# Kernel optimization log

Measured on AMD Instinct MI355X. Metric: run time of the kernel, lower is better.

## Reference

```python
import jax, jax.numpy as jnp
import numpy as np

BITS = 16          # number of histogram bins == number of spiking time steps
B, IN_DIM, HID = 16384, 784, 128


def setup_inputs() -> dict:
    key = jax.random.key(0)
    ks = jax.random.split(key, 9)
    dims = [(HID, IN_DIM), (HID, HID), (HID, HID), (IN_DIM, HID)]
    inp = {"features": jax.random.uniform(ks[0], (B, IN_DIM), jnp.float32)}
    for i, (o, d) in enumerate(dims):
        inp["W%d" % i] = jax.random.normal(ks[1 + i], (o, d), jnp.float32) * 0.05
        inp["b%d" % i] = jax.random.normal(ks[5 + i], (o,), jnp.float32) * 0.05
    # np.histogram_bin_edges(bins=16) -> 17 uniformly spaced edges per layer
    in_max = [1.0, 4.0, 4.0, 4.0]
    out_max = [4.0, 4.0, 4.0, 4.0]
    for i in range(4):
        inp["in_bins%d" % i] = jnp.linspace(0.0, in_max[i], BITS + 1, dtype=jnp.float32)
        inp["out_bins%d" % i] = jnp.linspace(0.0, out_max[i], BITS + 1, dtype=jnp.float32)
    return inp


def _spike(t):
    # output[output>1]=1; output[output<1]=0  (==1 stays 1)  -> (t >= 1)
    # totals[output==1] -= 1
    s = (t >= 1.0).astype(t.dtype)
    return s, t - s


def _forward(features, Ws, bs, in_bins, out_bins):
    h_in = [e[1] - e[0] for e in in_bins]    # uniform spike heights
    h_out = [e[1] - e[0] for e in out_bins]
    # set_up_weights: weight *= h_in; weight /= h_out (bias likewise)
    Weff = [Ws[l] * (h_in[l] / h_out[l]) for l in range(4)]
    beff = [bs[l] * (h_in[l] / h_out[l]) for l in range(4)]
    n = features.shape[0]
    # discretize: np.digitize(x, in_bins) - 1, then / 16.0 (non-differentiable)
    act = (jnp.digitize(jax.lax.stop_gradient(features), in_bins[0]) - 1).astype(features.dtype) / BITS
    t_in = jnp.zeros_like(features)                               # input-layer membrane
    totals = tuple(jnp.broadcast_to(beff[l], (n,) + beff[l].shape) for l in range(4))  # reset_totals: totals = bias
    out_acc = jnp.zeros((n, Weff[3].shape[0]), features.dtype)

    def step(carry, _):
        t_in, t0, t1, t2, t3, out = carry
        s_in, t_in = _spike(t_in + act)
        # process_layer: totals += sum(weight * spikes, axis=1) == spikes @ W.T
        s0, t0 = _spike(t0 + s_in @ Weff[0].T)
        s1, t1 = _spike(t1 + s0 @ Weff[1].T)
        s2, t2 = _spike(t2 + s1 @ Weff[2].T)
        s3, t3 = _spike(t3 + s2 @ Weff[3].T)
        return (t_in, t0, t1, t2, t3, out + s3), None

    carry, _ = jax.lax.scan(step, (t_in,) + totals + (out_acc,), None, length=BITS)
    out_spikes = carry[-1]
    # decoder_output_layer.reconstruct: spikes * (out_bins[1] - out_bins[0])
    return out_spikes * h_out[3]


def reference(features, W0, W1, W2, W3, b0, b1, b2, b3,
              in_bins0, in_bins1, in_bins2, in_bins3,
              out_bins0, out_bins1, out_bins2, out_bins3):
    return _forward(features,
                    [W0, W1, W2, W3], [b0, b1, b2, b3],
                    [in_bins0, in_bins1, in_bins2, in_bins3],
                    [out_bins0, out_bins1, out_bins2, out_bins3])
```

## Files before the change

### kernel.cpp

```cpp
#include <hip/hip_runtime.h>

#define IN_DIM 784
#define HID 128
#define NSTEP 16
#define BATCH 16384

constexpr int W0T_OFF = 0;
constexpr int W1T_OFF = W0T_OFF + IN_DIM*HID;
constexpr int W2T_OFF = W1T_OFF + HID*HID;
constexpr int W3T_OFF = W2T_OFF + HID*HID;
constexpr int B0_OFF  = W3T_OFF + HID*IN_DIM;
constexpr int B1_OFF  = B0_OFF + HID;
constexpr int B2_OFF  = B1_OFF + HID;
constexpr int B3_OFF  = B2_OFF + HID;
constexpr int WS_FLOATS = B3_OFF + IN_DIM;

constexpr int CHUNK_COLS = 32;
constexpr int CHUNK_F    = CHUNK_COLS * HID;
constexpr int NCHUNK     = 25;

__global__ __launch_bounds__(256) void prep_kernel(
    const float* __restrict__ W0, const float* __restrict__ b0,
    const float* __restrict__ W1, const float* __restrict__ b1,
    const float* __restrict__ W2, const float* __restrict__ b2,
    const float* __restrict__ W3, const float* __restrict__ b3,
    const float* __restrict__ ib0, const float* __restrict__ ob0,
    const float* __restrict__ ib1, const float* __restrict__ ob1,
    const float* __restrict__ ib2, const float* __restrict__ ob2,
    const float* __restrict__ ib3, const float* __restrict__ ob3,
    float* __restrict__ ws)
{
    int idx = blockIdx.x * 256 + threadIdx.x;
    if (idx >= WS_FLOATS) return;
    float r0 = (ib0[1] - ib0[0]) / (ob0[1] - ob0[0]);
    float r1 = (ib1[1] - ib1[0]) / (ob1[1] - ob1[0]);
    float r2 = (ib2[1] - ib2[0]) / (ob2[1] - ob2[0]);
    float r3 = (ib3[1] - ib3[0]) / (ob3[1] - ob3[0]);
    if (idx < W1T_OFF) {
        int t = idx;            int k = t >> 7, j = t & 127;
        ws[idx] = W0[j * IN_DIM + k] * r0;
    } else if (idx < W2T_OFF) {
        int t = idx - W1T_OFF;  int k = t >> 7, j = t & 127;
        ws[idx] = W1[j * HID + k] * r1;
    } else if (idx < W3T_OFF) {
        int t = idx - W2T_OFF;  int k = t >> 7, j = t & 127;
        ws[idx] = W2[j * HID + k] * r2;
    } else if (idx < B0_OFF) {
        int t = idx - W3T_OFF;  int k = t / IN_DIM, o = t % IN_DIM;
        ws[idx] = W3[o * HID + k] * r3;
    } else if (idx < B1_OFF) ws[idx] = b0[idx - B0_OFF] * r0;
    else if (idx < B2_OFF)   ws[idx] = b1[idx - B1_OFF] * r1;
    else if (idx < B3_OFF)   ws[idx] = b2[idx - B2_OFF] * r2;
    else                     ws[idx] = b3[idx - B3_OFF] * r3;
}

__global__ __launch_bounds__(256) void snn_main(
    const float* __restrict__ feat,
    const float* __restrict__ ws,
    const float* __restrict__ ib0,
    const float* __restrict__ ob3,
    float* __restrict__ out)
{
    __shared__ float smem[2 * CHUNK_F];

    const int tid  = threadIdx.x;
    const int lane = tid & 63;
    const int wid  = tid >> 6;
    const int sample = blockIdx.x * 4 + wid;

    const float* W0t = ws + W0T_OFF;
    const float* W1t = ws + W1T_OFF;
    const float* W2t = ws + W2T_OFF;
    const float* W3t = ws + W3T_OFF;
    const float* frow = feat + (size_t)sample * IN_DIM;

    float edge[16];
#pragma unroll
    for (int e = 0; e < 16; ++e) edge[e] = ib0[e + 1];

    {
        const float4* g4 = (const float4*)W0t;
        float4* lb = (float4*)smem;
#pragma unroll
        for (int i = 0; i < 4; ++i) lb[i * 256 + tid] = g4[i * 256 + tid];
    }
    __syncthreads();

    float2 C[16];
#pragma unroll
    for (int mv = 0; mv < 16; ++mv) C[mv] = make_float2(0.f, 0.f);

    for (int c = 0; c < NCHUNK; ++c) {
        float4 rg0, rg1, rg2, rg3;
        {
            const float4* g4 = (const float4*)W0t + (size_t)(c + 1) * (CHUNK_F / 4);
            rg0 = g4[0 * 256 + tid];
            rg1 = g4[1 * 256 + tid];
            rg2 = g4[2 * 256 + tid];
            rg3 = g4[3 * 256 + tid];
        }

        int col = c * CHUNK_COLS + (lane & 31);
        bool valid = col < IN_DIM;
        float x = frow[valid ? col : 0];
        int mm = 0;
#pragma unroll
        for (int e = 0; e < 16; ++e) mm += (x >= edge[e]) ? 1 : 0;
        if (!valid) mm = -1;

        const float2* bufp = (const float2*)(smem + (c & 1) * CHUNK_F);
#pragma unroll
        for (int mv = 1; mv <= 16; ++mv) {
            unsigned mk = (unsigned)__ballot(mm == mv);
            float2 ca = make_float2(0.f, 0.f), cb = make_float2(0.f, 0.f);
            while (mk) {
                int b0 = __builtin_ctz(mk); mk &= mk - 1;
                float2 w0 = bufp[b0 * 64 + lane];
                if (mk) {
                    int b1 = __builtin_ctz(mk); mk &= mk - 1;
                    float2 w1 = bufp[b1 * 64 + lane];
                    if (mk) {
                        int b2 = __builtin_ctz(mk); mk &= mk - 1;
                        float2 w2 = bufp[b2 * 64 + lane];
                        if (mk) {
                            int b3i = __builtin_ctz(mk); mk &= mk - 1;
                            float2 w3 = bufp[b3i * 64 + lane];
                            cb.x += w3.x; cb.y += w3.y;
                        }
                        ca.x += w2.x; ca.y += w2.y;
                    }
                    cb.x += w1.x; cb.y += w1.y;
                }
                ca.x += w0.x; ca.y += w0.y;
            }
            C[mv - 1].x += ca.x + cb.x;
            C[mv - 1].y += ca.y + cb.y;
        }

        if (c + 1 < NCHUNK) {
            float4* lb = (float4*)(smem + ((c + 1) & 1) * CHUNK_F);
            lb[0 * 256 + tid] = rg0;
            lb[1 * 256 + tid] = rg1;
            lb[2 * 256 + tid] = rg2;
            lb[3 * 256 + tid] = rg3;
        }
        __syncthreads();
    }

    float2 t0 = ((const float2*)(ws + B0_OFF))[lane];
    float2 t1 = ((const float2*)(ws + B1_OFF))[lane];
    float2 t2 = ((const float2*)(ws + B2_OFF))[lane];
    float4 t3[4], cnt[4];
    {
        const float4* b3v = (const float4*)(ws + B3_OFF);
#pragma unroll
        for (int r = 0; r < 3; ++r) t3[r] = b3v[r * 64 + lane];
        t3[3] = make_float4(0.f, 0.f, 0.f, 0.f);
        if (lane < 4) t3[3] = b3v[192 + lane];
#pragma unroll
        for (int r = 0; r < 4; ++r) cnt[r] = make_float4(0.f, 0.f, 0.f, 0.f);
    }

    for (int s = 1; s <= NSTEP; ++s) {
#pragma unroll
        for (int mv = 1; mv <= 16; ++mv) {
            if (((s * mv) & 15) < mv) { t0.x += C[mv - 1].x; t0.y += C[mv - 1].y; }
        }
        {
            bool px = (t0.x >= 1.0f), py = (t0.y >= 1.0f);
            unsigned long long mx = __ballot(px);
            unsigned long long my = __ballot(py);
            if (px) t0.x -= 1.0f;
            if (py) t0.y -= 1.0f;
            while (mx) {
                int b = __builtin_ctzll(mx); mx &= mx - 1;
                const float2* colp = (const float2*)(W1t + (2 * b) * HID);
                float2 w = colp[lane]; t1.x += w.x; t1.y += w.y;
            }
            while (my) {
                int b = __builtin_ctzll(my); my &= my - 1;
                const float2* colp = (const float2*)(W1t + (2 * b + 1) * HID);
                float2 w = colp[lane]; t1.x += w.x; t1.y += w.y;
            }
        }
        {
            bool px = (t1.x >= 1.0f), py = (t1.y >= 1.0f);
            unsigned long long mx = __ballot(px);
            unsigned long long my = __ballot(py);
            if (px) t1.x -= 1.0f;
            if (py) t1.y -= 1.0f;
            while (mx) {
                int b = __builtin_ctzll(mx); mx &= mx - 1;
                const float2* colp = (const float2*)(W2t + (2 * b) * HID);
                float2 w = colp[lane]; t2.x += w.x; t2.y += w.y;
            }
            while (my) {
                int b = __builtin_ctzll(my); my &= my - 1;
                const float2* colp = (const float2*)(W2t + (2 * b + 1) * HID);
                float2 w = colp[lane]; t2.x += w.x; t2.y += w.y;
            }
        }
        {
            bool px = (t2.x >= 1.0f), py = (t2.y >= 1.0f);
            unsigned long long mx = __ballot(px);
            unsigned long long my = __ballot(py);
            if (px) t2.x -= 1.0f;
            if (py) t2.y -= 1.0f;
            while (mx) {
                int b = __builtin_ctzll(mx); mx &= mx - 1;
                const float4* colp = (const float4*)(W3t + (2 * b) * IN_DIM);
#pragma unroll
                for (int r = 0; r < 3; ++r) {
                    float4 w = colp[r * 64 + lane];
                    t3[r].x += w.x; t3[r].y += w.y; t3[r].z += w.z; t3[r].w += w.w;
                }
                if (lane < 4) {
                    float4 w = colp[192 + lane];
                    t3[3].x += w.x; t3[3].y += w.y; t3[3].z += w.z; t3[3].w += w.w;
                }
            }
            while (my) {
                int b = __builtin_ctzll(my); my &= my - 1;
                const float4* colp = (const float4*)(W3t + (2 * b + 1) * IN_DIM);
#pragma unroll
                for (int r = 0; r < 3; ++r) {
                    float4 w = colp[r * 64 + lane];
                    t3[r].x += w.x; t3[r].y += w.y; t3[r].z += w.z; t3[r].w += w.w;
                }
                if (lane < 4) {
                    float4 w = colp[192 + lane];
                    t3[3].x += w.x; t3[3].y += w.y; t3[3].z += w.z; t3[3].w += w.w;
                }
            }
        }
#pragma unroll
        for (int r = 0; r < 4; ++r) {
            if (t3[r].x >= 1.0f) { t3[r].x -= 1.0f; cnt[r].x += 1.0f; }
            if (t3[r].y >= 1.0f) { t3[r].y -= 1.0f; cnt[r].y += 1.0f; }
            if (t3[r].z >= 1.0f) { t3[r].z -= 1.0f; cnt[r].z += 1.0f; }
            if (t3[r].w >= 1.0f) { t3[r].w -= 1.0f; cnt[r].w += 1.0f; }
        }
    }

    const float h = ob3[1] - ob3[0];
    float4* orow = (float4*)(out + (size_t)sample * IN_DIM);
#pragma unroll
    for (int r = 0; r < 3; ++r)
        orow[r * 64 + lane] = make_float4(cnt[r].x * h, cnt[r].y * h, cnt[r].z * h, cnt[r].w * h);
    if (lane < 4)
        orow[192 + lane] = make_float4(cnt[3].x * h, cnt[3].y * h, cnt[3].z * h, cnt[3].w * h);
}

extern "C" void kernel_launch(void* const* d_in, const int* in_sizes, int n_in,
                              void* d_out, int out_size, void* d_ws, size_t ws_size,
                              hipStream_t stream)
{
    const float* feat = (const float*)d_in[0];
    const float* W0  = (const float*)d_in[1];
    const float* b0  = (const float*)d_in[2];
    const float* W1  = (const float*)d_in[3];
    const float* b1  = (const float*)d_in[4];
    const float* W2  = (const float*)d_in[5];
    const float* b2  = (const float*)d_in[6];
    const float* W3  = (const float*)d_in[7];
    const float* b3  = (const float*)d_in[8];
    const float* ib0 = (const float*)d_in[9];
    const float* ob0 = (const float*)d_in[10];
    const float* ib1 = (const float*)d_in[11];
    const float* ob1 = (const float*)d_in[12];
    const float* ib2 = (const float*)d_in[13];
    const float* ob2 = (const float*)d_in[14];
    const float* ib3 = (const float*)d_in[15];
    const float* ob3 = (const float*)d_in[16];
    float* ws  = (float*)d_ws;
    float* op  = (float*)d_out;

    prep_kernel<<<(WS_FLOATS + 255) / 256, 256, 0, stream>>>(
        W0, b0, W1, b1, W2, b2, W3, b3,
        ib0, ob0, ib1, ob1, ib2, ob2, ib3, ob3, ws);

    snn_main<<<BATCH / 4, 256, 0, stream>>>(feat, ws, ib0, ob3, op);
}
```

Measured before the change: 436.9 us.

## Use 512-thread blocks and batch spike-driven weight gathers with scalar indices

The block grows from 4 to 8 waves, one sample per wave, so each shared-memory W0 chunk is reused by twice as many samples and per-thread staging loads are halved. In the hidden and output layers, spike-driven column gathers are unrolled four or two at a time with split accumulators, and readfirstlane keeps the column indices scalar. Several global loads can then be in flight at once instead of a serial load-add chain. Vector ext types replace the per-component float2/float4 arithmetic. The cost is higher register pressure and larger blocks, which may reduce occupancy or scheduling flexibility.

```diff
diff --git a/kernel.cpp b/kernel.cpp
--- a/kernel.cpp
+++ b/kernel.cpp
@@ -4,6 +4,9 @@
 #define HID 128
 #define NSTEP 16
 #define BATCH 16384
+
+typedef float v2f __attribute__((ext_vector_type(2)));
+typedef float v4f __attribute__((ext_vector_type(4)));
 
 constexpr int W0T_OFF = 0;
 constexpr int W1T_OFF = W0T_OFF + IN_DIM*HID;
@@ -18,6 +21,9 @@
 constexpr int CHUNK_COLS = 32;
 constexpr int CHUNK_F    = CHUNK_COLS * HID;
 constexpr int NCHUNK     = 25;
+
+constexpr int TPB   = 512;
+constexpr int WAVES = TPB / 64;
 
 __global__ __launch_bounds__(256) void prep_kernel(
     const float* __restrict__ W0, const float* __restrict__ b0,
@@ -54,7 +60,7 @@
     else                     ws[idx] = b3[idx - B3_OFF] * r3;
 }
 
-__global__ __launch_bounds__(256) void snn_main(
+__global__ __launch_bounds__(TPB) void snn_main(
     const float* __restrict__ feat,
     const float* __restrict__ ws,
     const float* __restrict__ ib0,
@@ -66,7 +72,7 @@
     const int tid  = threadIdx.x;
     const int lane = tid & 63;
     const int wid  = tid >> 6;
-    const int sample = blockIdx.x * 4 + wid;
+    const int sample = blockIdx.x * WAVES + wid;
 
     const float* W0t = ws + W0T_OFF;
     const float* W1t = ws + W1T_OFF;
@@ -82,22 +88,20 @@
         const float4* g4 = (const float4*)W0t;
         float4* lb = (float4*)smem;
 #pragma unroll
-        for (int i = 0; i < 4; ++i) lb[i * 256 + tid] = g4[i * 256 + tid];
+        for (int i = 0; i < 2; ++i) lb[i * TPB + tid] = g4[i * TPB + tid];
     }
     __syncthreads();
 
-    float2 C[16];
-#pragma unroll
-    for (int mv = 0; mv < 16; ++mv) C[mv] = make_float2(0.f, 0.f);
+    v2f C[16];
+#pragma unroll
+    for (int mv = 0; mv < 16; ++mv) C[mv] = (v2f)(0.f);
 
     for (int c = 0; c < NCHUNK; ++c) {
-        float4 rg0, rg1, rg2, rg3;
+        float4 rg0, rg1;
         {
             const float4* g4 = (const float4*)W0t + (size_t)(c + 1) * (CHUNK_F / 4);
-            rg0 = g4[0 * 256 + tid];
-            rg1 = g4[1 * 256 + tid];
-            rg2 = g4[2 * 256 + tid];
-            rg3 = g4[3 * 256 + tid];
+            rg0 = g4[0 * TPB + tid];
+            rg1 = g4[1 * TPB + tid];
         }
 
         int col = c * CHUNK_COLS + (lane & 31);
@@ -108,63 +112,60 @@
         for (int e = 0; e < 16; ++e) mm += (x >= edge[e]) ? 1 : 0;
         if (!valid) mm = -1;
 
-        const float2* bufp = (const float2*)(smem + (c & 1) * CHUNK_F);
+        const v2f* bufp = (const v2f*)(smem + (c & 1) * CHUNK_F);
 #pragma unroll
         for (int mv = 1; mv <= 16; ++mv) {
             unsigned mk = (unsigned)__ballot(mm == mv);
-            float2 ca = make_float2(0.f, 0.f), cb = make_float2(0.f, 0.f);
+            v2f ca = (v2f)(0.f), cb = (v2f)(0.f);
             while (mk) {
                 int b0 = __builtin_ctz(mk); mk &= mk - 1;
-                float2 w0 = bufp[b0 * 64 + lane];
+                v2f w0 = bufp[b0 * 64 + lane];
                 if (mk) {
                     int b1 = __builtin_ctz(mk); mk &= mk - 1;
-                    float2 w1 = bufp[b1 * 64 + lane];
+                    v2f w1 = bufp[b1 * 64 + lane];
                     if (mk) {
                         int b2 = __builtin_ctz(mk); mk &= mk - 1;
-                        float2 w2 = bufp[b2 * 64 + lane];
+                        v2f w2 = bufp[b2 * 64 + lane];
                         if (mk) {
                             int b3i = __builtin_ctz(mk); mk &= mk - 1;
-                            float2 w3 = bufp[b3i * 64 + lane];
-                            cb.x += w3.x; cb.y += w3.y;
-                        }
-                        ca.x += w2.x; ca.y += w2.y;
-                    }
-                    cb.x += w1.x; cb.y += w1.y;
-                }
-                ca.x += w0.x; ca.y += w0.y;
-            }
-            C[mv - 1].x += ca.x + cb.x;
-            C[mv - 1].y += ca.y + cb.y;
+                            v2f w3 = bufp[b3i * 64 + lane];
+                            cb += w3;
+                        }
+                        ca += w2;
+                    }
+                    cb += w1;
+                }
+                ca += w0;
+            }
+            C[mv - 1] += ca + cb;
         }
 
         if (c + 1 < NCHUNK) {
             float4* lb = (float4*)(smem + ((c + 1) & 1) * CHUNK_F);
-            lb[0 * 256 + tid] = rg0;
-            lb[1 * 256 + tid] = rg1;
-            lb[2 * 256 + tid] = rg2;
-            lb[3 * 256 + tid] = rg3;
+            lb[0 * TPB + tid] = rg0;
+            lb[1 * TPB + tid] = rg1;
         }
         __syncthreads();
     }
 
-    float2 t0 = ((const float2*)(ws + B0_OFF))[lane];
-    float2 t1 = ((const float2*)(ws + B1_OFF))[lane];
-    float2 t2 = ((const float2*)(ws + B2_OFF))[lane];
-    float4 t3[4], cnt[4];
+    v2f t0 = ((const v2f*)(ws + B0_OFF))[lane];
+    v2f t1 = ((const v2f*)(ws + B1_OFF))[lane];
+    v2f t2 = ((const v2f*)(ws + B2_OFF))[lane];
+    v4f t3[4], cnt[4];
     {
-        const float4* b3v = (const float4*)(ws + B3_OFF);
+        const v4f* b3v = (const v4f*)(ws + B3_OFF);
 #pragma unroll
         for (int r = 0; r < 3; ++r) t3[r] = b3v[r * 64 + lane];
-        t3[3] = make_float4(0.f, 0.f, 0.f, 0.f);
+        t3[3] = (v4f)(0.f);
         if (lane < 4) t3[3] = b3v[192 + lane];
 #pragma unroll
-        for (int r = 0; r < 4; ++r) cnt[r] = make_float4(0.f, 0.f, 0.f, 0.f);
+        for (int r = 0; r < 4; ++r) cnt[r] = (v4f)(0.f);
     }
 
     for (int s = 1; s <= NSTEP; ++s) {
 #pragma unroll
         for (int mv = 1; mv <= 16; ++mv) {
-            if (((s * mv) & 15) < mv) { t0.x += C[mv - 1].x; t0.y += C[mv - 1].y; }
+            if (((s * mv) & 15) < mv) t0 += C[mv - 1];
         }
         {
             bool px = (t0.x >= 1.0f), py = (t0.y >= 1.0f);
@@ -172,16 +173,48 @@
             unsigned long long my = __ballot(py);
             if (px) t0.x -= 1.0f;
             if (py) t0.y -= 1.0f;
+            v2f ca = (v2f)(0.f), cb = (v2f)(0.f);
             while (mx) {
-                int b = __builtin_ctzll(mx); mx &= mx - 1;
-                const float2* colp = (const float2*)(W1t + (2 * b) * HID);
-                float2 w = colp[lane]; t1.x += w.x; t1.y += w.y;
+                int b0 = __builtin_amdgcn_readfirstlane(__builtin_ctzll(mx)); mx &= mx - 1;
+                v2f w0 = ((const v2f*)(W1t + (2 * b0) * HID))[lane];
+                if (mx) {
+                    int b1 = __builtin_amdgcn_readfirstlane(__builtin_ctzll(mx)); mx &= mx - 1;
+                    v2f w1 = ((const v2f*)(W1t + (2 * b1) * HID))[lane];
+                    if (mx) {
+                        int b2 = __builtin_amdgcn_readfirstlane(__builtin_ctzll(mx)); mx &= mx - 1;
+                        v2f w2 = ((const v2f*)(W1t + (2 * b2) * HID))[lane];
+                        if (mx) {
+                            int b3i = __builtin_amdgcn_readfirstlane(__builtin_ctzll(mx)); mx &= mx - 1;
+                            v2f w3 = ((const v2f*)(W1t + (2 * b3i) * HID))[lane];
+                            cb += w3;
+                        }
+                        ca += w2;
+                    }
+                    cb += w1;
+                }
+                ca += w0;
             }
             while (my) {
-                int b = __builtin_ctzll(my); my &= my - 1;
-                const float2* colp = (const float2*)(W1t + (2 * b + 1) * HID);
-                float2 w = colp[lane]; t1.x += w.x; t1.y += w.y;
-            }
+                int b0 = __builtin_amdgcn_readfirstlane(__builtin_ctzll(my)); my &= my - 1;
+                v2f w0 = ((const v2f*)(W1t + (2 * b0 + 1) * HID))[lane];
+                if (my) {
+                    int b1 = __builtin_amdgcn_readfirstlane(__builtin_ctzll(my)); my &= my - 1;
+                    v2f w1 = ((const v2f*)(W1t + (2 * b1 + 1) * HID))[lane];
+                    if (my) {
+                        int b2 = __builtin_amdgcn_readfirstlane(__builtin_ctzll(my)); my &= my - 1;
+                        v2f w2 = ((const v2f*)(W1t + (2 * b2 + 1) * HID))[lane];
+                        if (my) {
+                            int b3i = __builtin_amdgcn_readfirstlane(__builtin_ctzll(my)); my &= my - 1;
+                            v2f w3 = ((const v2f*)(W1t + (2 * b3i + 1) * HID))[lane];
+                            cb += w3;
+                        }
+                        ca += w2;
+                    }
+                    cb += w1;
+                }
+                ca += w0;
+            }
+            t1 += ca + cb;
         }
         {
             bool px = (t1.x >= 1.0f), py = (t1.y >= 1.0f);
@@ -189,16 +222,48 @@
             unsigned long long my = __ballot(py);
             if (px) t1.x -= 1.0f;
             if (py) t1.y -= 1.0f;
+            v2f ca = (v2f)(0.f), cb = (v2f)(0.f);
             while (mx) {
-                int b = __builtin_ctzll(mx); mx &= mx - 1;
-                const float2* colp = (const float2*)(W2t + (2 * b) * HID);
-                float2 w = colp[lane]; t2.x += w.x; t2.y += w.y;
+                int b0 = __builtin_amdgcn_readfirstlane(__builtin_ctzll(mx)); mx &= mx - 1;
+                v2f w0 = ((const v2f*)(W2t + (2 * b0) * HID))[lane];
+                if (mx) {
+                    int b1 = __builtin_amdgcn_readfirstlane(__builtin_ctzll(mx)); mx &= mx - 1;
+                    v2f w1 = ((const v2f*)(W2t + (2 * b1) * HID))[lane];
+                    if (mx) {
+                        int b2 = __builtin_amdgcn_readfirstlane(__builtin_ctzll(mx)); mx &= mx - 1;
+                        v2f w2 = ((const v2f*)(W2t + (2 * b2) * HID))[lane];
+                        if (mx) {
+                            int b3i = __builtin_amdgcn_readfirstlane(__builtin_ctzll(mx)); mx &= mx - 1;
+                            v2f w3 = ((const v2f*)(W2t + (2 * b3i) * HID))[lane];
+                            cb += w3;
+                        }
+                        ca += w2;
+                    }
+                    cb += w1;
+                }
+                ca += w0;
             }
             while (my) {
-                int b = __builtin_ctzll(my); my &= my - 1;
-                const float2* colp = (const float2*)(W2t + (2 * b + 1) * HID);
-                float2 w = colp[lane]; t2.x += w.x; t2.y += w.y;
-            }
+                int b0 = __builtin_amdgcn_readfirstlane(__builtin_ctzll(my)); my &= my - 1;
+                v2f w0 = ((const v2f*)(W2t + (2 * b0 + 1) * HID))[lane];
+                if (my) {
+                    int b1 = __builtin_amdgcn_readfirstlane(__builtin_ctzll(my)); my &= my - 1;
+                    v2f w1 = ((const v2f*)(W2t + (2 * b1 + 1) * HID))[lane];
+                    if (my) {
+                        int b2 = __builtin_amdgcn_readfirstlane(__builtin_ctzll(my)); my &= my - 1;
+                        v2f w2 = ((const v2f*)(W2t + (2 * b2 + 1) * HID))[lane];
+                        if (my) {
+                            int b3i = __builtin_amdgcn_readfirstlane(__builtin_ctzll(my)); my &= my - 1;
+                            v2f w3 = ((const v2f*)(W2t + (2 * b3i + 1) * HID))[lane];
+                            cb += w3;
+                        }
+                        ca += w2;
+                    }
+                    cb += w1;
+                }
+                ca += w0;
+            }
+            t2 += ca + cb;
         }
         {
             bool px = (t2.x >= 1.0f), py = (t2.y >= 1.0f);
@@ -207,30 +272,36 @@
             if (px) t2.x -= 1.0f;
             if (py) t2.y -= 1.0f;
             while (mx) {
-                int b = __builtin_ctzll(mx); mx &= mx - 1;
-                const float4* colp = (const float4*)(W3t + (2 * b) * IN_DIM);
-#pragma unroll
-                for (int r = 0; r < 3; ++r) {
-                    float4 w = colp[r * 64 + lane];
-                    t3[r].x += w.x; t3[r].y += w.y; t3[r].z += w.z; t3[r].w += w.w;
-                }
-                if (lane < 4) {
-                    float4 w = colp[192 + lane];
-                    t3[3].x += w.x; t3[3].y += w.y; t3[3].z += w.z; t3[3].w += w.w;
-                }
+                int b0 = __builtin_amdgcn_readfirstlane(__builtin_ctzll(mx)); mx &= mx - 1;
+                const v4f* c0 = (const v4f*)(W3t + (2 * b0) * IN_DIM);
+                v4f x0 = c0[lane], x1 = c0[64 + lane], x2 = c0[128 + lane];
+                v4f x3 = c0[192 + (lane & 3)];
+                if (mx) {
+                    int b1 = __builtin_amdgcn_readfirstlane(__builtin_ctzll(mx)); mx &= mx - 1;
+                    const v4f* c1 = (const v4f*)(W3t + (2 * b1) * IN_DIM);
+                    v4f y0 = c1[lane], y1 = c1[64 + lane], y2 = c1[128 + lane];
+                    v4f y3 = c1[192 + (lane & 3)];
+                    t3[0] += y0; t3[1] += y1; t3[2] += y2;
+                    if (lane < 4) t3[3] += y3;
+                }
+                t3[0] += x0; t3[1] += x1; t3[2] += x2;
+                if (lane < 4) t3[3] += x3;
             }
             while (my) {
-                int b = __builtin_ctzll(my); my &= my - 1;
-                const float4* colp = (const float4*)(W3t + (2 * b + 1) * IN_DIM);
-#pragma unroll
-                for (int r = 0; r < 3; ++r) {
-                    float4 w = colp[r * 64 + lane];
-                    t3[r].x += w.x; t3[r].y += w.y; t3[r].z += w.z; t3[r].w += w.w;
-                }
-                if (lane < 4) {
-                    float4 w = colp[192 + lane];
-                    t3[3].x += w.x; t3[3].y += w.y; t3[3].z += w.z; t3[3].w += w.w;
-                }
+                int b0 = __builtin_amdgcn_readfirstlane(__builtin_ctzll(my)); my &= my - 1;
+                const v4f* c0 = (const v4f*)(W3t + (2 * b0 + 1) * IN_DIM);
+                v4f x0 = c0[lane], x1 = c0[64 + lane], x2 = c0[128 + lane];
+                v4f x3 = c0[192 + (lane & 3)];
+                if (my) {
+                    int b1 = __builtin_amdgcn_readfirstlane(__builtin_ctzll(my)); my &= my - 1;
+                    const v4f* c1 = (const v4f*)(W3t + (2 * b1 + 1) * IN_DIM);
+                    v4f y0 = c1[lane], y1 = c1[64 + lane], y2 = c1[128 + lane];
+                    v4f y3 = c1[192 + (lane & 3)];
+                    t3[0] += y0; t3[1] += y1; t3[2] += y2;
+                    if (lane < 4) t3[3] += y3;
+                }
+                t3[0] += x0; t3[1] += x1; t3[2] += x2;
+                if (lane < 4) t3[3] += x3;
             }
         }
 #pragma unroll
@@ -243,12 +314,12 @@
     }
 
     const float h = ob3[1] - ob3[0];
-    float4* orow = (float4*)(out + (size_t)sample * IN_DIM);
+    v4f* orow = (v4f*)(out + (size_t)sample * IN_DIM);
 #pragma unroll
     for (int r = 0; r < 3; ++r)
-        orow[r * 64 + lane] = make_float4(cnt[r].x * h, cnt[r].y * h, cnt[r].z * h, cnt[r].w * h);
+        orow[r * 64 + lane] = cnt[r] * h;
     if (lane < 4)
-        orow[192 + lane] = make_float4(cnt[3].x * h, cnt[3].y * h, cnt[3].z * h, cnt[3].w * h);
+        orow[192 + lane] = cnt[3] * h;
 }
 
 extern "C" void kernel_launch(void* const* d_in, const int* in_sizes, int n_in,
@@ -279,5 +350,5 @@
         W0, b0, W1, b1, W2, b2, W3, b3,
         ib0, ob0, ib1, ob1, ib2, ob2, ib3, ob3, ws);
 
-    snn_main<<<BATCH / 4, 256, 0, stream>>>(feat, ws, ib0, ob3, op);
+    snn_main<<<BATCH / WAVES, TPB, 0, stream>>>(feat, ws, ib0, ob3, op);
 }
```

New measurement: 412.9 us. 5.5% less time.
